# Optimization experiments

Hardware: AMD Instinct MI355X
Metric: run time of the kernel (lower is better)

Reference implementation:

```python
import jax, jax.numpy as jnp
import numpy as np

NUM_BEAMS = 2


def setup_inputs() -> dict:
    key = jax.random.key(0)
    ks = jax.random.split(key, 5)
    B, T, H, E, F = 128, 32, 768, 4, 3072
    x = jax.random.normal(ks[0], (B, T, H), dtype=jnp.float32)
    Wg = jax.random.normal(ks[1], (E, H), dtype=jnp.float32) * (1.0 / np.sqrt(H))
    W1 = jax.random.normal(ks[2], (E, H, F), dtype=jnp.float32) * (1.0 / np.sqrt(H))
    b1 = jnp.zeros((E, F), dtype=jnp.float32)
    W2 = jax.random.normal(ks[3], (E, F, H), dtype=jnp.float32) * (1.0 / np.sqrt(F))
    b2 = jnp.zeros((E, H), dtype=jnp.float32)
    return {"x": x, "Wg": Wg, "W1": W1, "b1": b1, "W2": W2, "b2": b2}


def reference(x, Wg, W1, b1, W2, b2):
    B, T, H = x.shape
    E = Wg.shape[0]
    nb = NUM_BEAMS
    # ---- forward_gate: mask is all-ones, so masked mean == mean over tokens ----
    x_avg = jnp.mean(x, axis=1)                          # [B, H]
    logits_gate = x_avg @ Wg.T                           # [B, E]
    prob_gate = jax.nn.softmax(logits_gate, axis=-1)     # [B, E]
    # ---- importance auxiliary loss (torch.std uses ddof=1) ----
    importance = jnp.sum(prob_gate, axis=0)              # [E]
    importance_loss = (jnp.std(importance, ddof=1) / jnp.mean(importance)) ** 2
    # ---- beam search, first layer: exp(log(p)) == p, top-k per row ----
    current_scores = jnp.exp(jnp.log(prob_gate))         # == prob_gate (kept for fidelity)
    topk_values, gate_idx = jax.lax.top_k(current_scores, nb)   # [B, nb]
    beam_scores = topk_values.reshape(nb * B)            # row-major flatten, matches .view
    expert_route = gate_idx.reshape(nb * B)[:, None]     # [B*nb, 1]
    beam_idx = jnp.arange(nb * B)
    current_expert_select = expert_route[:, -1]          # [B*nb]
    # ---- first layer: replicate x and scores along beam dim (interleaved) ----
    x_rep = jnp.repeat(x, nb, axis=0)                    # [B*nb, T, H]
    scores_rep = jnp.repeat(prob_gate, nb, axis=0)       # [B*nb, E]
    # input_x = x_rep[beam_idx] is identity here (beam_idx == arange)
    # ---- forward_expert_ffn: run ALL experts, mask+combine with gate prob ----
    h1 = jnp.einsum('bth,ehf->betf', x_rep, W1) + b1[None, :, None, :]
    h1 = jax.nn.gelu(h1, approximate=False)              # torch GELU is exact erf form
    cand = jnp.einsum('betf,efh->beth', h1, W2) + b2[None, :, None, :]  # [B*nb, E, T, H]
    weight = scores_rep * jax.nn.one_hot(current_expert_select, E, dtype=scores_rep.dtype)
    output = jnp.einsum('beth,be->bth', cand, weight)    # weighted sum over experts
    return output, beam_scores, expert_route, beam_idx, importance_loss
```

## Files before the change

### kernel.cpp

```cpp
#include <hip/hip_runtime.h>
#include <math.h>

typedef _Float16 f16;
typedef _Float16 f16x8 __attribute__((ext_vector_type(8)));
typedef float f32x4 __attribute__((ext_vector_type(4)));

#define Bn 128
#define Tn 32
#define Hn 768
#define En 4
#define Fn 3072
#define Rn 256
#define MAXT4 67

static constexpr size_t OUT_ELEMS  = (size_t)Rn*Tn*Hn;
static constexpr size_t SCORES_OFF = OUT_ELEMS;
static constexpr size_t ROUTE_OFF  = OUT_ELEMS + Rn;
static constexpr size_t BIDX_OFF   = OUT_ELEMS + 2*Rn;
static constexpr size_t LOSS_OFF   = OUT_ELEMS + 3*Rn;

#define WS_WSF    0u
#define WS_ROUTE  4096u
#define WS_GRP    8192u
#define WS_X16    16384u
#define WS_W1T    (WS_X16 + 2u*Bn*Tn*Hn)
#define WS_W2T    (WS_W1T + 2u*En*Hn*Fn)
#define WS_H1     (WS_W2T + 2u*En*Fn*Hn)

#define GLOAD16(g, l) __builtin_amdgcn_global_load_lds( \
    (const __attribute__((address_space(1))) unsigned int*)(g), \
    (__attribute__((address_space(3))) unsigned int*)(l), 16, 0, 0)

__device__ __forceinline__ float fast_gelu(float v) {
  float s = v * 0.70710678118f;
  float a = fabsf(s);
  float t = 1.0f / (1.0f + 0.3275911f * a);
  float y = t*(0.254829592f + t*(-0.284496736f + t*(1.421413741f +
            t*(-1.453152027f + t*1.061405429f))));
  float er = 1.0f - y * __expf(-a*a);
  er = (s < 0.0f) ? -er : er;
  return 0.5f * v * (1.0f + er);
}

__global__ __launch_bounds__(256) void gate_kernel(
    const float* __restrict__ x, const float* __restrict__ Wg,
    float* __restrict__ out, float* __restrict__ wsf, int* __restrict__ route,
    f16* __restrict__ x16)
{
  const int b = blockIdx.x;
  const int tid = threadIdx.x;
  const int w = tid >> 6, l = tid & 63;
  __shared__ float pacc[4][4];
  float a0=0.f, a1=0.f, a2=0.f, a3=0.f;
  const float* xb = x   + (size_t)b*Tn*Hn + (size_t)(w*8)*Hn;
  f16*         xh = x16 + (size_t)b*Tn*Hn + (size_t)(w*8)*Hn;
  #pragma unroll
  for (int k = 0; k < 12; ++k) {
    const int h = l + 64*k;
    const float w0 = Wg[0*Hn+h], w1 = Wg[1*Hn+h], w2 = Wg[2*Hn+h], w3 = Wg[3*Hn+h];
    #pragma unroll
    for (int t = 0; t < 8; ++t) {
      float v = xb[t*Hn + h];
      xh[t*Hn + h] = (f16)v;
      a0 += v*w0; a1 += v*w1; a2 += v*w2; a3 += v*w3;
    }
  }
  #pragma unroll
  for (int o = 32; o > 0; o >>= 1) {
    a0 += __shfl_down(a0,o); a1 += __shfl_down(a1,o);
    a2 += __shfl_down(a2,o); a3 += __shfl_down(a3,o);
  }
  if (l == 0) { pacc[w][0]=a0; pacc[w][1]=a1; pacc[w][2]=a2; pacc[w][3]=a3; }
  __syncthreads();
  if (tid == 0) {
    float lg[4];
    #pragma unroll
    for (int e = 0; e < 4; ++e)
      lg[e] = (pacc[0][e]+pacc[1][e]+pacc[2][e]+pacc[3][e]) * (1.0f/Tn);
    float m = fmaxf(fmaxf(lg[0],lg[1]), fmaxf(lg[2],lg[3]));
    float p[4]; float s = 0.f;
    #pragma unroll
    for (int e = 0; e < 4; ++e) { p[e] = expf(lg[e]-m); s += p[e]; }
    float inv = 1.f/s;
    #pragma unroll
    for (int e = 0; e < 4; ++e) { p[e] *= inv; wsf[b*4+e] = p[e]; }
    int i1 = 0;
    #pragma unroll
    for (int e = 1; e < 4; ++e) if (p[e] > p[i1]) i1 = e;
    int i2 = (i1 == 0) ? 1 : 0;
    #pragma unroll
    for (int e = 0; e < 4; ++e) if (e != i1 && p[e] > p[i2]) i2 = e;
    int idx[2] = {i1, i2};
    #pragma unroll
    for (int k = 0; k < 2; ++k) {
      int r = 2*b + k;
      float pv = p[idx[k]];
      wsf[512 + r] = pv;
      route[r] = idx[k];
      out[SCORES_OFF + r] = pv;
      out[ROUTE_OFF  + r] = (float)idx[k];
      out[BIDX_OFF   + r] = (float)r;
    }
  }
}

__global__ __launch_bounds__(64) void loss_kernel(
    const float* __restrict__ wsf, float* __restrict__ out)
{
  const int l = threadIdx.x;
  float i0=0.f,i1=0.f,i2=0.f,i3=0.f;
  for (int b = l; b < Bn; b += 64) {
    i0 += wsf[b*4+0]; i1 += wsf[b*4+1]; i2 += wsf[b*4+2]; i3 += wsf[b*4+3];
  }
  #pragma unroll
  for (int o = 32; o > 0; o >>= 1) {
    i0 += __shfl_down(i0,o); i1 += __shfl_down(i1,o);
    i2 += __shfl_down(i2,o); i3 += __shfl_down(i3,o);
  }
  if (l == 0) {
    float mean = 0.25f*(i0+i1+i2+i3);
    float d0=i0-mean, d1=i1-mean, d2=i2-mean, d3=i3-mean;
    float var = (d0*d0+d1*d1+d2*d2+d3*d3) * (1.f/3.f);
    out[LOSS_OFF] = var / (mean*mean);
  }
}

__global__ __launch_bounds__(64) void group_kernel(
    const int* __restrict__ route, int* __restrict__ grp)
{
  const int l = threadIdx.x;
  int cnt = 0;
  if (l < 4) { for (int r = 0; r < Rn; ++r) cnt += (route[r] == l); }
  int c0 = __shfl(cnt, 0), c1 = __shfl(cnt, 1), c2 = __shfl(cnt, 2), c3 = __shfl(cnt, 3);
  int off = (l >= 1 ? c0 : 0) + (l >= 2 ? c1 : 0) + (l >= 3 ? c2 : 0);
  if (l < 4) {
    int p = off;
    for (int r = 0; r < Rn; ++r) if (route[r] == l) grp[384 + p++] = r;
  }
  if (l == 0) {
    int cs[4] = {c0, c1, c2, c3};
    int os[4] = {0, c0, c0+c1, c0+c1+c2};
    int nt4 = 0;
    for (int e = 0; e < 4; ++e) {
      for (int s = 0; s < cs[e]; s += 4) {
        int nb = cs[e] - s; if (nb > 4) nb = 4;
        grp[8+nt4*3+0] = e; grp[8+nt4*3+1] = os[e]+s; grp[8+nt4*3+2] = nb;
        ++nt4;
      }
    }
    grp[0] = nt4;
  }
}

__global__ __launch_bounds__(256) void transcvt_kernel(
    const float* __restrict__ W1s, const float* __restrict__ W2s,
    f16* __restrict__ d1, f16* __restrict__ d2)
{
  __shared__ f16 t[64][74];
  int bid = blockIdx.x;
  const float* s; f16* d; int R, C, rc;
  if (bid < 2304) { s = W1s; d = d1; R = Hn; C = Fn; rc = bid; }
  else            { s = W2s; d = d2; R = Fn; C = Hn; rc = bid - 2304; }
  const int e = rc / 576; rc -= e*576;
  const int nx = C >> 6;
  const int cy = rc / nx, cx = rc - cy*nx;
  const int r0 = cy*64, c0 = cx*64;
  s += (size_t)e*R*C;
  d += (size_t)e*R*C;
  const int tid = threadIdx.x;
  const int i  = tid >> 2;
  const int j0 = (tid & 3) * 16;
  #pragma unroll
  for (int q = 0; q < 16; q += 4) {
    float4 v = *(const float4*)(s + (size_t)(r0+i)*C + c0 + j0 + q);
    t[i][j0+q+0]=(f16)v.x; t[i][j0+q+1]=(f16)v.y; t[i][j0+q+2]=(f16)v.z; t[i][j0+q+3]=(f16)v.w;
  }
  __syncthreads();
  f16 o[16];
  #pragma unroll
  for (int q = 0; q < 16; ++q) o[q] = t[j0+q][i];
  *(uint4*)(d + (size_t)(c0+i)*R + r0 + j0)     = *(uint4*)&o[0];
  *(uint4*)(d + (size_t)(c0+i)*R + r0 + j0 + 8) = *(uint4*)&o[8];
}

template<int KD, int ND, int BN, int NWAVE, bool G1>
__global__ __launch_bounds__(NWAVE*64, G1 ? 4 : 2) void gemm_kernel(
    const f16* __restrict__ A16, const f16* __restrict__ B16,
    const float* __restrict__ bias, f16* __restrict__ oh,
    float* __restrict__ of, const int* __restrict__ grp,
    const float* __restrict__ wsf)
{
  constexpr int NWY  = BN / 64;
  constexpr int NY   = ND / BN;
  constexpr int NT   = KD / 32;
  constexpr int NTHR = NWAVE * 64;
  constexpr int GL_A = 512 / NTHR;
  constexpr int GL_B = (BN*4) / NTHR;
  constexpr int NLD  = GL_A + GL_B;
  constexpr int BUFSZ = 8192 + BN*64;
  constexpr int TPR  = NWAVE * 2;
  static_assert(NT % 3 == 0, "NT%3");

  const int ntiles = grp[0];
  const int tix = blockIdx.x / NY;
  const int ny  = blockIdx.x % NY;
  if (tix >= ntiles) return;
  const int e      = grp[8+tix*3+0];
  const int bstart = grp[8+tix*3+1];
  const int nb     = grp[8+tix*3+2];
  const int n0     = ny * BN;
  const int tid    = threadIdx.x;
  const int lane   = tid & 63;
  const int w      = tid >> 6;

  extern __shared__ __align__(16) char smem[];

  const f16* asrc[GL_A];
  #pragma unroll
  for (int i = 0; i < GL_A; ++i) {
    const int U   = w*(GL_A*64) + i*64 + lane;
    const int row = U >> 2;
    const int gu  = (U & 3) ^ ((U >> 3) & 3);
    int slot = row >> 5; if (slot >= nb) slot = nb - 1;
    const int beam = grp[384 + bstart + slot];
    const size_t rbase = (G1 ? (size_t)(beam>>1)*Tn : (size_t)beam*Tn) + (row & 31);
    asrc[i] = A16 + rbase*(size_t)KD + gu*8;
  }
  const f16* bsrc[GL_B];
  #pragma unroll
  for (int i = 0; i < GL_B; ++i) {
    const int U   = w*(GL_B*64) + i*64 + lane;
    const int row = U >> 2;
    const int gu  = (U & 3) ^ ((U >> 3) & 3);
    bsrc[i] = B16 + (size_t)e*ND*KD + (size_t)(n0 + row)*KD + gu*8;
  }

  const int wm = w / NWY, wn = w % NWY;
  const int lr = lane & 15, lk = lane >> 4;
  const int rowA0 = wm*64;
  const int rowB0 = wn*64;
  const int ub = (lk ^ ((lr >> 1) & 3)) << 4;

  f32x4 acc[4][4];
  #pragma unroll
  for (int i=0;i<4;++i)
    #pragma unroll
    for (int j=0;j<4;++j) acc[i][j] = (f32x4){0.f,0.f,0.f,0.f};

  auto STAGE = [&](int bsel, int kt2) {
    char* Ad = smem + bsel*BUFSZ + (w*(GL_A*64))*16;
    #pragma unroll
    for (int i = 0; i < GL_A; ++i) GLOAD16(asrc[i] + kt2*32, Ad + i*1024);
    char* Bd = smem + bsel*BUFSZ + 8192 + (w*(GL_B*64))*16;
    #pragma unroll
    for (int i = 0; i < GL_B; ++i) GLOAD16(bsrc[i] + kt2*32, Bd + i*1024);
  };

  auto TILE = [&](int k, int b, bool dost, int vmc) {
    const char* Ab = smem + b*BUFSZ;
    const char* Bb = Ab + 8192;
    f16x8 af[4], bf[4];
    #pragma unroll
    for (int mi=0;mi<4;++mi)
      af[mi] = *(const f16x8*)(Ab + (rowA0 + mi*16 + lr)*64 + ub);
    #pragma unroll
    for (int ni=0;ni<4;++ni)
      bf[ni] = *(const f16x8*)(Bb + (rowB0 + ni*16 + lr)*64 + ub);
    if (dost) STAGE((b+2)%3, k+2);
    __builtin_amdgcn_sched_barrier(0);
    __builtin_amdgcn_s_barrier();
    __builtin_amdgcn_sched_barrier(0);
    asm volatile("s_waitcnt lgkmcnt(0)" ::: "memory");
    __builtin_amdgcn_sched_barrier(0);
    __builtin_amdgcn_s_setprio(1);
    #pragma unroll
    for (int mi=0;mi<4;++mi)
      #pragma unroll
      for (int ni=0;ni<4;++ni)
        acc[mi][ni] = __builtin_amdgcn_mfma_f32_16x16x32_f16(af[mi], bf[ni], acc[mi][ni], 0, 0, 0);
    __builtin_amdgcn_s_setprio(0);
    if (vmc > 0)       asm volatile("s_waitcnt vmcnt(%0)" :: "i"(NLD) : "memory");
    else if (vmc == 0) asm volatile("s_waitcnt vmcnt(0)" ::: "memory");
    __builtin_amdgcn_sched_barrier(0);
    __builtin_amdgcn_s_barrier();
    __builtin_amdgcn_sched_barrier(0);
  };

  STAGE(0, 0);
  STAGE(1, 1);
  asm volatile("s_waitcnt vmcnt(%0)" :: "i"(NLD) : "memory");
  __builtin_amdgcn_sched_barrier(0);
  __builtin_amdgcn_s_barrier();
  __builtin_amdgcn_sched_barrier(0);

  {
    int b = 0;
    for (int k = 0; k < NT-2; ++k) {
      TILE(k, b, true, NLD);
      b = (b+1)%3;
    }
    TILE(NT-2, b, false, 0);
    b = (b+1)%3;
    TILE(NT-1, b, false, -1);
  }

  const int nvalid = nb * Tn;
  char* cst = smem;
  float bvals[4];
  if (G1) {
    #pragma unroll
    for (int ni=0;ni<4;++ni) bvals[ni] = bias[e*ND + n0 + rowB0 + ni*16 + lr];
  }
  #pragma unroll
  for (int mi=0;mi<4;++mi){
    #pragma unroll
    for (int j=0;j<4;++j){
      const int m = rowA0 + mi*16 + (lane>>4)*4 + j;
      const int m7 = m & 7;
      #pragma unroll
      for (int ni=0;ni<4;++ni){
        const int n = rowB0 + ni*16 + lr;
        if (G1) {
          float v = acc[mi][ni][j] + bvals[ni];
          *(f16*)(cst + m*512 + (((n>>3)^m7)<<4) + (n&7)*2) = (f16)fast_gelu(v);
        } else {
          *(float*)(cst + m*512 + (((n>>2)^m7)<<4) + (n&3)*4) = acc[mi][ni][j];
        }
      }
    }
  }
  __syncthreads();
  {
    const int u  = tid & 31;
    const int tr = tid >> 5;
    float4 b4;
    if (!G1) b4 = *(const float4*)(bias + e*ND + n0 + u*4);
    #pragma unroll
    for (int it = 0; it < 128/TPR; ++it) {
      const int rl = it*TPR + tr;
      if (rl < nvalid) {
        const int beam = grp[384 + bstart + (rl>>5)];
        if (G1) {
          uint4 v = *(const uint4*)(cst + rl*512 + (((u&24)|((u&7)^(rl&7)))<<4));
          *(uint4*)(oh + ((size_t)beam*Tn + (rl&31))*(size_t)ND + n0 + u*8) = v;
        } else {
          const float sc = wsf[512 + beam];
          float4 v = *(const float4*)(cst + rl*512 + (((u&24)|((u&7)^(rl&7)))<<4));
          v.x = (v.x + b4.x)*sc; v.y = (v.y + b4.y)*sc;
          v.z = (v.z + b4.z)*sc; v.w = (v.w + b4.w)*sc;
          *(float4*)(of + ((size_t)beam*Tn + (rl&31))*(size_t)Hn + n0 + u*4) = v;
        }
      }
    }
  }
}

extern "C" void kernel_launch(void* const* d_in, const int* in_sizes, int n_in,
                              void* d_out, int out_size, void* d_ws, size_t ws_size,
                              hipStream_t stream)
{
  const float* x  = (const float*)d_in[0];
  const float* Wg = (const float*)d_in[1];
  const float* W1 = (const float*)d_in[2];
  const float* b1 = (const float*)d_in[3];
  const float* W2 = (const float*)d_in[4];
  const float* b2 = (const float*)d_in[5];
  float* out = (float*)d_out;
  char* ws = (char*)d_ws;
  float* wsf  = (float*)(ws + WS_WSF);
  int*   route= (int*)(ws + WS_ROUTE);
  int*   grp  = (int*)(ws + WS_GRP);
  f16*   x16  = (f16*)(ws + WS_X16);
  f16*   w1t  = (f16*)(ws + WS_W1T);
  f16*   w2t  = (f16*)(ws + WS_W2T);
  f16*   h1   = (f16*)(ws + WS_H1);

  gate_kernel<<<Bn, 256, 0, stream>>>(x, Wg, out, wsf, route, x16);
  group_kernel<<<1, 64, 0, stream>>>(route, grp);
  loss_kernel<<<1, 64, 0, stream>>>(wsf, out);
  transcvt_kernel<<<4608, 256, 0, stream>>>(W1, W2, w1t, w2t);

  auto g1 = gemm_kernel<Hn, Fn, 256, 8, true>;
  auto g2 = gemm_kernel<Fn, Hn, 128, 4, false>;
  const int sm1 = 3*(8192 + 256*64);
  const int sm2 = 65536;
  hipFuncSetAttribute((const void*)g1, hipFuncAttributeMaxDynamicSharedMemorySize, sm1);
  hipFuncSetAttribute((const void*)g2, hipFuncAttributeMaxDynamicSharedMemorySize, sm2);
  g1<<<MAXT4*12, 512, sm1, stream>>>(x16, w1t, b1, h1, nullptr, grp, wsf);
  g2<<<MAXT4*6,  256, sm2, stream>>>(h1, w2t, b2, nullptr, out, grp, wsf);
}
```

Measured before the change: 204.7 us.

## Shrink GEMM tiles, switch to double-buffered pipeline, reorder grid by column tile

Both grouped-expert GEMMs now use 256-thread blocks with smaller N tiles (128 for the first, 64 for the second), so more blocks launch and more can be resident per CU at lower LDS use. The three-stage prefetch pipeline with priority hints becomes a simpler two-buffer scheme that waits for all loads before every barrier. Block indexing now iterates row tiles fastest, so blocks sharing a weight column tile run close together. The epilogue is split into two halves to fit the smaller shared buffer. In exchange, less load latency is hidden per block and each A tile is re-read from global memory more times.

```diff
diff --git a/kernel.cpp b/kernel.cpp
--- a/kernel.cpp
+++ b/kernel.cpp
@@ -183,27 +183,21 @@
   *(uint4*)(d + (size_t)(c0+i)*R + r0 + j0 + 8) = *(uint4*)&o[8];
 }
 
-template<int KD, int ND, int BN, int NWAVE, bool G1>
-__global__ __launch_bounds__(NWAVE*64, G1 ? 4 : 2) void gemm_kernel(
+template<int KD, int ND, int BN, int NI, bool G1>
+__global__ __launch_bounds__(256, 4) void gemm_kernel(
     const f16* __restrict__ A16, const f16* __restrict__ B16,
     const float* __restrict__ bias, f16* __restrict__ oh,
     float* __restrict__ of, const int* __restrict__ grp,
     const float* __restrict__ wsf)
 {
-  constexpr int NWY  = BN / 64;
-  constexpr int NY   = ND / BN;
   constexpr int NT   = KD / 32;
-  constexpr int NTHR = NWAVE * 64;
-  constexpr int GL_A = 512 / NTHR;
-  constexpr int GL_B = (BN*4) / NTHR;
-  constexpr int NLD  = GL_A + GL_B;
-  constexpr int BUFSZ = 8192 + BN*64;
-  constexpr int TPR  = NWAVE * 2;
-  static_assert(NT % 3 == 0, "NT%3");
+  constexpr int GL_B = BN / 64;
+  constexpr int BUFSZ = (128 + BN) * 64;
+  static_assert(NT % 2 == 0, "NT even");
 
   const int ntiles = grp[0];
-  const int tix = blockIdx.x / NY;
-  const int ny  = blockIdx.x % NY;
+  const int ny  = blockIdx.x / MAXT4;
+  const int tix = blockIdx.x % MAXT4;
   if (tix >= ntiles) return;
   const int e      = grp[8+tix*3+0];
   const int bstart = grp[8+tix*3+1];
@@ -215,10 +209,10 @@
 
   extern __shared__ __align__(16) char smem[];
 
-  const f16* asrc[GL_A];
-  #pragma unroll
-  for (int i = 0; i < GL_A; ++i) {
-    const int U   = w*(GL_A*64) + i*64 + lane;
+  const f16* asrc[2];
+  #pragma unroll
+  for (int i = 0; i < 2; ++i) {
+    const int U   = w*128 + i*64 + lane;
     const int row = U >> 2;
     const int gu  = (U & 3) ^ ((U >> 3) & 3);
     int slot = row >> 5; if (slot >= nb) slot = nb - 1;
@@ -235,123 +229,118 @@
     bsrc[i] = B16 + (size_t)e*ND*KD + (size_t)(n0 + row)*KD + gu*8;
   }
 
-  const int wm = w / NWY, wn = w % NWY;
+  const int wm = w >> 1, wn = w & 1;
   const int lr = lane & 15, lk = lane >> 4;
   const int rowA0 = wm*64;
-  const int rowB0 = wn*64;
+  const int rowB0 = wn*(NI*16);
   const int ub = (lk ^ ((lr >> 1) & 3)) << 4;
 
-  f32x4 acc[4][4];
+  f32x4 acc[4][NI];
   #pragma unroll
   for (int i=0;i<4;++i)
     #pragma unroll
-    for (int j=0;j<4;++j) acc[i][j] = (f32x4){0.f,0.f,0.f,0.f};
+    for (int j=0;j<NI;++j) acc[i][j] = (f32x4){0.f,0.f,0.f,0.f};
 
   auto STAGE = [&](int bsel, int kt2) {
-    char* Ad = smem + bsel*BUFSZ + (w*(GL_A*64))*16;
-    #pragma unroll
-    for (int i = 0; i < GL_A; ++i) GLOAD16(asrc[i] + kt2*32, Ad + i*1024);
+    char* Ad = smem + bsel*BUFSZ + (w*128)*16;
+    #pragma unroll
+    for (int i = 0; i < 2; ++i) GLOAD16(asrc[i] + kt2*32, Ad + i*1024);
     char* Bd = smem + bsel*BUFSZ + 8192 + (w*(GL_B*64))*16;
     #pragma unroll
     for (int i = 0; i < GL_B; ++i) GLOAD16(bsrc[i] + kt2*32, Bd + i*1024);
   };
 
-  auto TILE = [&](int k, int b, bool dost, int vmc) {
+  auto TILE = [&](int k, int b) {
     const char* Ab = smem + b*BUFSZ;
     const char* Bb = Ab + 8192;
-    f16x8 af[4], bf[4];
+    f16x8 af[4], bf[NI];
     #pragma unroll
     for (int mi=0;mi<4;++mi)
       af[mi] = *(const f16x8*)(Ab + (rowA0 + mi*16 + lr)*64 + ub);
     #pragma unroll
-    for (int ni=0;ni<4;++ni)
+    for (int ni=0;ni<NI;++ni)
       bf[ni] = *(const f16x8*)(Bb + (rowB0 + ni*16 + lr)*64 + ub);
-    if (dost) STAGE((b+2)%3, k+2);
-    __builtin_amdgcn_sched_barrier(0);
-    __builtin_amdgcn_s_barrier();
-    __builtin_amdgcn_sched_barrier(0);
+    if (k + 1 < NT) STAGE(b ^ 1, k + 1);
     asm volatile("s_waitcnt lgkmcnt(0)" ::: "memory");
     __builtin_amdgcn_sched_barrier(0);
-    __builtin_amdgcn_s_setprio(1);
     #pragma unroll
     for (int mi=0;mi<4;++mi)
       #pragma unroll
-      for (int ni=0;ni<4;++ni)
+      for (int ni=0;ni<NI;++ni)
         acc[mi][ni] = __builtin_amdgcn_mfma_f32_16x16x32_f16(af[mi], bf[ni], acc[mi][ni], 0, 0, 0);
-    __builtin_amdgcn_s_setprio(0);
-    if (vmc > 0)       asm volatile("s_waitcnt vmcnt(%0)" :: "i"(NLD) : "memory");
-    else if (vmc == 0) asm volatile("s_waitcnt vmcnt(0)" ::: "memory");
+    asm volatile("s_waitcnt vmcnt(0)" ::: "memory");
     __builtin_amdgcn_sched_barrier(0);
     __builtin_amdgcn_s_barrier();
     __builtin_amdgcn_sched_barrier(0);
   };
 
   STAGE(0, 0);
-  STAGE(1, 1);
-  asm volatile("s_waitcnt vmcnt(%0)" :: "i"(NLD) : "memory");
+  asm volatile("s_waitcnt vmcnt(0)" ::: "memory");
   __builtin_amdgcn_sched_barrier(0);
   __builtin_amdgcn_s_barrier();
   __builtin_amdgcn_sched_barrier(0);
 
-  {
-    int b = 0;
-    for (int k = 0; k < NT-2; ++k) {
-      TILE(k, b, true, NLD);
-      b = (b+1)%3;
-    }
-    TILE(NT-2, b, false, 0);
-    b = (b+1)%3;
-    TILE(NT-1, b, false, -1);
+  for (int k = 0; k < NT; k += 2) {
+    TILE(k,   0);
+    TILE(k+1, 1);
   }
 
   const int nvalid = nb * Tn;
   char* cst = smem;
-  float bvals[4];
-  if (G1) {
-    #pragma unroll
-    for (int ni=0;ni<4;++ni) bvals[ni] = bias[e*ND + n0 + rowB0 + ni*16 + lr];
-  }
-  #pragma unroll
-  for (int mi=0;mi<4;++mi){
-    #pragma unroll
-    for (int j=0;j<4;++j){
-      const int m = rowA0 + mi*16 + (lane>>4)*4 + j;
-      const int m7 = m & 7;
+  float bvals[NI];
+  #pragma unroll
+  for (int ni=0;ni<NI;++ni)
+    if (G1) bvals[ni] = bias[e*ND + n0 + rowB0 + ni*16 + lr];
+
+  #pragma unroll
+  for (int h = 0; h < 2; ++h) {
+    if (wm == h) {
       #pragma unroll
-      for (int ni=0;ni<4;++ni){
-        const int n = rowB0 + ni*16 + lr;
-        if (G1) {
-          float v = acc[mi][ni][j] + bvals[ni];
-          *(f16*)(cst + m*512 + (((n>>3)^m7)<<4) + (n&7)*2) = (f16)fast_gelu(v);
-        } else {
-          *(float*)(cst + m*512 + (((n>>2)^m7)<<4) + (n&3)*4) = acc[mi][ni][j];
+      for (int mi=0;mi<4;++mi){
+        #pragma unroll
+        for (int j=0;j<4;++j){
+          const int m = mi*16 + (lane>>4)*4 + j;
+          const int m7 = m & 7;
+          #pragma unroll
+          for (int ni=0;ni<NI;++ni){
+            const int n = rowB0 + ni*16 + lr;
+            if (G1) {
+              float v = acc[mi][ni][j] + bvals[ni];
+              *(f16*)(cst + m*512 + (((n>>3)^m7)<<4) + (n&7)*2) = (f16)fast_gelu(v);
+            } else {
+              *(float*)(cst + m*512 + (((n>>2)^m7)<<4) + (n&3)*4) = acc[mi][ni][j];
+            }
+          }
         }
       }
     }
-  }
-  __syncthreads();
-  {
-    const int u  = tid & 31;
-    const int tr = tid >> 5;
-    float4 b4;
-    if (!G1) b4 = *(const float4*)(bias + e*ND + n0 + u*4);
-    #pragma unroll
-    for (int it = 0; it < 128/TPR; ++it) {
-      const int rl = it*TPR + tr;
-      if (rl < nvalid) {
-        const int beam = grp[384 + bstart + (rl>>5)];
-        if (G1) {
-          uint4 v = *(const uint4*)(cst + rl*512 + (((u&24)|((u&7)^(rl&7)))<<4));
-          *(uint4*)(oh + ((size_t)beam*Tn + (rl&31))*(size_t)ND + n0 + u*8) = v;
-        } else {
-          const float sc = wsf[512 + beam];
-          float4 v = *(const float4*)(cst + rl*512 + (((u&24)|((u&7)^(rl&7)))<<4));
-          v.x = (v.x + b4.x)*sc; v.y = (v.y + b4.y)*sc;
-          v.z = (v.z + b4.z)*sc; v.w = (v.w + b4.w)*sc;
-          *(float4*)(of + ((size_t)beam*Tn + (rl&31))*(size_t)Hn + n0 + u*4) = v;
+    __syncthreads();
+    {
+      const int u  = tid & 15;
+      const int tr = tid >> 4;
+      float4 b4;
+      if (!G1) b4 = *(const float4*)(bias + e*ND + n0 + u*4);
+      #pragma unroll
+      for (int it = 0; it < 4; ++it) {
+        const int rl = it*16 + tr;
+        const int r  = h*64 + rl;
+        if (r < nvalid) {
+          const int beam = grp[384 + bstart + (r>>5)];
+          const char* src = cst + rl*512 + ((u ^ (rl&7))<<4);
+          if (G1) {
+            uint4 v = *(const uint4*)src;
+            *(uint4*)(oh + ((size_t)beam*Tn + (r&31))*(size_t)ND + n0 + u*8) = v;
+          } else {
+            const float sc = wsf[512 + beam];
+            float4 v = *(const float4*)src;
+            v.x = (v.x + b4.x)*sc; v.y = (v.y + b4.y)*sc;
+            v.z = (v.z + b4.z)*sc; v.w = (v.w + b4.w)*sc;
+            *(float4*)(of + ((size_t)beam*Tn + (r&31))*(size_t)Hn + n0 + u*4) = v;
+          }
         }
       }
     }
+    __syncthreads();
   }
 }
 
@@ -380,12 +369,11 @@
   loss_kernel<<<1, 64, 0, stream>>>(wsf, out);
   transcvt_kernel<<<4608, 256, 0, stream>>>(W1, W2, w1t, w2t);
 
-  auto g1 = gemm_kernel<Hn, Fn, 256, 8, true>;
-  auto g2 = gemm_kernel<Fn, Hn, 128, 4, false>;
-  const int sm1 = 3*(8192 + 256*64);
-  const int sm2 = 65536;
-  hipFuncSetAttribute((const void*)g1, hipFuncAttributeMaxDynamicSharedMemorySize, sm1);
-  hipFuncSetAttribute((const void*)g2, hipFuncAttributeMaxDynamicSharedMemorySize, sm2);
-  g1<<<MAXT4*12, 512, sm1, stream>>>(x16, w1t, b1, h1, nullptr, grp, wsf);
-  g2<<<MAXT4*6,  256, sm2, stream>>>(h1, w2t, b2, nullptr, out, grp, wsf);
-}
+  auto g1 = gemm_kernel<Hn, Fn, 128, 4, true>;
+  auto g2 = gemm_kernel<Fn, Hn,  64, 2, false>;
+  const int smB = 32768;
+  hipFuncSetAttribute((const void*)g1, hipFuncAttributeMaxDynamicSharedMemorySize, smB);
+  hipFuncSetAttribute((const void*)g2, hipFuncAttributeMaxDynamicSharedMemorySize, smB);
+  g1<<<24*MAXT4, 256, smB, stream>>>(x16, w1t, b1, h1, nullptr, grp, wsf);
+  g2<<<12*MAXT4, 256, smB, stream>>>(h1, w2t, b2, nullptr, out, grp, wsf);
+}
```

Result: slower. 270.5 us (+32.2%).

## Use 256x256 tiles with 8-beam groups and split-phase pipeline for first GEMM

Applied to the files above, without the earlier changes.

The first expert GEMM gets its own kernel that takes 256-row tiles (up to 8 beams per group) by 256 columns, with a K-step of 64 and double-buffered 128KB LDS. Each wave computes a 128x64 sub-tile in four MFMA phases, with loads for the next stages interleaved between the phases. The grouping kernel now emits separate 8-beam and 4-beam tile lists for the two GEMMs. This cuts how often the W1 tiles are reloaded and raises arithmetic intensity, but it costs more padding waste for partial groups and lower occupancy from the large LDS footprint.

```diff
diff --git a/kernel.cpp b/kernel.cpp
--- a/kernel.cpp
+++ b/kernel.cpp
@@ -11,6 +11,7 @@
 #define En 4
 #define Fn 3072
 #define Rn 256
+#define MAXT8 35
 #define MAXT4 67
 
 static constexpr size_t OUT_ELEMS  = (size_t)Rn*Tn*Hn;
@@ -30,6 +31,9 @@
 #define GLOAD16(g, l) __builtin_amdgcn_global_load_lds( \
     (const __attribute__((address_space(1))) unsigned int*)(g), \
     (__attribute__((address_space(3))) unsigned int*)(l), 16, 0, 0)
+
+#define SBAR()  __builtin_amdgcn_s_barrier()
+#define SCHED() __builtin_amdgcn_sched_barrier(0)
 
 __device__ __forceinline__ float fast_gelu(float v) {
   float s = v * 0.70710678118f;
@@ -140,15 +144,21 @@
   if (l == 0) {
     int cs[4] = {c0, c1, c2, c3};
     int os[4] = {0, c0, c0+c1, c0+c1+c2};
-    int nt4 = 0;
+    int nt8 = 0, nt4 = 0;
     for (int e = 0; e < 4; ++e) {
+      for (int s = 0; s < cs[e]; s += 8) {
+        int nb = cs[e] - s; if (nb > 8) nb = 8;
+        grp[8+nt8*3+0] = e; grp[8+nt8*3+1] = os[e]+s; grp[8+nt8*3+2] = nb;
+        ++nt8;
+      }
       for (int s = 0; s < cs[e]; s += 4) {
         int nb = cs[e] - s; if (nb > 4) nb = 4;
-        grp[8+nt4*3+0] = e; grp[8+nt4*3+1] = os[e]+s; grp[8+nt4*3+2] = nb;
+        grp[128+nt4*3+0] = e; grp[128+nt4*3+1] = os[e]+s; grp[128+nt4*3+2] = nb;
         ++nt4;
       }
     }
-    grp[0] = nt4;
+    grp[0] = nt8;
+    grp[1] = nt4;
   }
 }
 
@@ -183,12 +193,170 @@
   *(uint4*)(d + (size_t)(c0+i)*R + r0 + j0 + 8) = *(uint4*)&o[8];
 }
 
-template<int KD, int ND, int BN, int NWAVE, bool G1>
-__global__ __launch_bounds__(NWAVE*64, G1 ? 4 : 2) void gemm_kernel(
+__global__ __launch_bounds__(512) void gemm1_kernel(
     const f16* __restrict__ A16, const f16* __restrict__ B16,
     const float* __restrict__ bias, f16* __restrict__ oh,
-    float* __restrict__ of, const int* __restrict__ grp,
-    const float* __restrict__ wsf)
+    const int* __restrict__ grp)
+{
+  constexpr int KD = Hn, ND = Fn, NT = KD/64, NY = Fn/256;
+  const int ntiles = grp[0];
+  const int tix = blockIdx.x / NY;
+  const int ny  = blockIdx.x % NY;
+  if (tix >= ntiles) return;
+  const int e      = grp[8+tix*3+0];
+  const int bstart = grp[8+tix*3+1];
+  const int nb     = grp[8+tix*3+2];
+  const int n0     = ny * 256;
+  const int tid    = threadIdx.x;
+  const int lane   = tid & 63;
+  const int w      = tid >> 6;
+
+  extern __shared__ __align__(16) char smem[];
+
+  const f16* aS[2][2];
+  const f16* bS[2][2];
+  #pragma unroll
+  for (int h = 0; h < 2; ++h) {
+    #pragma unroll
+    for (int i = 0; i < 2; ++i) {
+      const int U = w*128 + i*64 + lane;
+      const int r128 = U >> 3;
+      const int gu = (U & 7) ^ (r128 & 7);
+      const int rowA = h*128 + r128;
+      int slot = rowA >> 5; if (slot >= nb) slot = nb - 1;
+      const int beam = grp[384 + bstart + slot];
+      aS[h][i] = A16 + ((size_t)(beam>>1)*Tn + (rowA&31))*(size_t)KD + gu*8;
+      bS[h][i] = B16 + (size_t)e*ND*KD + (size_t)(n0 + h*128 + r128)*KD + gu*8;
+    }
+  }
+
+  const int wm = w >> 2, wn = w & 3;
+  const int lr = lane & 15, lk = lane >> 4;
+  const int r7 = lr & 7;
+  const char* Abase = smem + wm*16384;
+  const char* Bbase = smem + 32768 + (wn>>1)*16384;
+  const int cb = (wn & 1) * 64;
+
+  f32x4 acc[8][4];
+  #pragma unroll
+  for (int i=0;i<8;++i)
+    #pragma unroll
+    for (int j=0;j<4;++j) acc[i][j] = (f32x4){0.f,0.f,0.f,0.f};
+
+  auto STAGE_A = [&](int d, int h, int kt) {
+    char* dst = smem + d*65536 + h*16384 + w*2048;
+    GLOAD16(aS[h][0] + kt*64, dst);
+    GLOAD16(aS[h][1] + kt*64, dst + 1024);
+  };
+  auto STAGE_B = [&](int d, int h, int kt) {
+    char* dst = smem + d*65536 + 32768 + h*16384 + w*2048;
+    GLOAD16(bS[h][0] + kt*64, dst);
+    GLOAD16(bS[h][1] + kt*64, dst + 1024);
+  };
+
+  f16x8 af[4][2], bf[2][2][2];
+
+#define LDA(MH, MI, KS) \
+  *(const f16x8*)(Abase + d*65536 + ((MH)*64 + (MI)*16 + lr)*128 + (((KS)*4+lk)^r7)*16)
+#define LDB(NH, NI, KS) \
+  *(const f16x8*)(Bbase + d*65536 + (cb + (NH)*32 + (NI)*16 + lr)*128 + (((KS)*4+lk)^r7)*16)
+#define MFMA16(MH, NH) \
+  __builtin_amdgcn_s_setprio(1); \
+  _Pragma("unroll") \
+  for (int mi=0;mi<4;++mi) \
+    _Pragma("unroll") \
+    for (int ni=0;ni<2;++ni) \
+      _Pragma("unroll") \
+      for (int ks=0;ks<2;++ks) \
+        acc[(MH)*4+mi][(NH)*2+ni] = __builtin_amdgcn_mfma_f32_16x16x32_f16( \
+            af[mi][ks], bf[NH][ni][ks], acc[(MH)*4+mi][(NH)*2+ni], 0, 0, 0); \
+  __builtin_amdgcn_s_setprio(0);
+
+  STAGE_A(0,0,0); STAGE_A(0,1,0); STAGE_B(0,0,0); STAGE_B(0,1,0);
+  STAGE_A(1,0,1); STAGE_A(1,1,1); STAGE_B(1,0,1); STAGE_B(1,1,1);
+  asm volatile("s_waitcnt vmcnt(8)" ::: "memory");
+  SCHED(); SBAR(); SCHED();
+
+  for (int kt = 0; kt < NT; ++kt) {
+    const int d = kt & 1;
+    const bool st = (kt + 2 < NT);
+    #pragma unroll
+    for (int mi=0;mi<4;++mi) { af[mi][0] = LDA(0,mi,0); af[mi][1] = LDA(0,mi,1); }
+    #pragma unroll
+    for (int ni=0;ni<2;++ni) { bf[0][ni][0] = LDB(0,ni,0); bf[0][ni][1] = LDB(0,ni,1); }
+    SBAR(); SCHED();
+    asm volatile("s_waitcnt lgkmcnt(0)" ::: "memory");
+    SCHED();
+    MFMA16(0,0);
+    SBAR(); SCHED();
+    #pragma unroll
+    for (int ni=0;ni<2;++ni) { bf[1][ni][0] = LDB(1,ni,0); bf[1][ni][1] = LDB(1,ni,1); }
+    SBAR(); SCHED();
+    asm volatile("s_waitcnt lgkmcnt(0)" ::: "memory");
+    SCHED();
+    MFMA16(0,1);
+    SBAR(); SCHED();
+    #pragma unroll
+    for (int mi=0;mi<4;++mi) { af[mi][0] = LDA(1,mi,0); af[mi][1] = LDA(1,mi,1); }
+    if (st) { STAGE_B(d, 0, kt+2); STAGE_B(d, 1, kt+2); }
+    SBAR(); SCHED();
+    asm volatile("s_waitcnt lgkmcnt(0)" ::: "memory");
+    SCHED();
+    MFMA16(1,0);
+    SBAR(); SCHED();
+    if (st) { STAGE_A(d, 0, kt+2); STAGE_A(d, 1, kt+2); }
+    SBAR(); SCHED();
+    MFMA16(1,1);
+    if (st)                asm volatile("s_waitcnt vmcnt(8)" ::: "memory");
+    else if (kt + 1 < NT)  asm volatile("s_waitcnt vmcnt(0)" ::: "memory");
+    SCHED(); SBAR(); SCHED();
+  }
+#undef LDA
+#undef LDB
+#undef MFMA16
+
+  __syncthreads();
+  const int nvalid = nb * Tn;
+  char* cst = smem;
+  float bvals[4];
+  #pragma unroll
+  for (int ni=0;ni<4;++ni) bvals[ni] = bias[e*ND + n0 + wn*64 + ni*16 + lr];
+
+  #pragma unroll
+  for (int mi=0;mi<8;++mi){
+    #pragma unroll
+    for (int j=0;j<4;++j){
+      const int m = wm*128 + mi*16 + (lane>>4)*4 + j;
+      const int m7 = m & 7;
+      #pragma unroll
+      for (int ni=0;ni<4;++ni){
+        const int n = wn*64 + ni*16 + lr;
+        float v = acc[mi][ni][j] + bvals[ni];
+        *(f16*)(cst + m*512 + (((n>>3)^m7)<<4) + (n&7)*2) = (f16)fast_gelu(v);
+      }
+    }
+  }
+  __syncthreads();
+  {
+    const int u  = tid & 31;
+    const int tr = tid >> 5;
+    #pragma unroll
+    for (int it = 0; it < 16; ++it) {
+      const int r = it*16 + tr;
+      if (r < nvalid) {
+        const int beam = grp[384 + bstart + (r>>5)];
+        uint4 v = *(const uint4*)(cst + r*512 + (((u&24)|((u&7)^(r&7)))<<4));
+        *(uint4*)(oh + ((size_t)beam*Tn + (r&31))*(size_t)ND + n0 + u*8) = v;
+      }
+    }
+  }
+}
+
+template<int KD, int ND, int BN, int NWAVE>
+__global__ __launch_bounds__(NWAVE*64, 2) void gemm2_kernel(
+    const f16* __restrict__ A16, const f16* __restrict__ B16,
+    const float* __restrict__ bias, float* __restrict__ of,
+    const int* __restrict__ grp, const float* __restrict__ wsf)
 {
   constexpr int NWY  = BN / 64;
   constexpr int NY   = ND / BN;
@@ -201,13 +369,13 @@
   constexpr int TPR  = NWAVE * 2;
   static_assert(NT % 3 == 0, "NT%3");
 
-  const int ntiles = grp[0];
+  const int ntiles = grp[1];
   const int tix = blockIdx.x / NY;
   const int ny  = blockIdx.x % NY;
   if (tix >= ntiles) return;
-  const int e      = grp[8+tix*3+0];
-  const int bstart = grp[8+tix*3+1];
-  const int nb     = grp[8+tix*3+2];
+  const int e      = grp[128+tix*3+0];
+  const int bstart = grp[128+tix*3+1];
+  const int nb     = grp[128+tix*3+2];
   const int n0     = ny * BN;
   const int tid    = threadIdx.x;
   const int lane   = tid & 63;
@@ -223,7 +391,7 @@
     const int gu  = (U & 3) ^ ((U >> 3) & 3);
     int slot = row >> 5; if (slot >= nb) slot = nb - 1;
     const int beam = grp[384 + bstart + slot];
-    const size_t rbase = (G1 ? (size_t)(beam>>1)*Tn : (size_t)beam*Tn) + (row & 31);
+    const size_t rbase = (size_t)beam*Tn + (row & 31);
     asrc[i] = A16 + rbase*(size_t)KD + gu*8;
   }
   const f16* bsrc[GL_B];
@@ -267,11 +435,9 @@
     for (int ni=0;ni<4;++ni)
       bf[ni] = *(const f16x8*)(Bb + (rowB0 + ni*16 + lr)*64 + ub);
     if (dost) STAGE((b+2)%3, k+2);
-    __builtin_amdgcn_sched_barrier(0);
-    __builtin_amdgcn_s_barrier();
-    __builtin_amdgcn_sched_barrier(0);
+    SCHED(); SBAR(); SCHED();
     asm volatile("s_waitcnt lgkmcnt(0)" ::: "memory");
-    __builtin_amdgcn_sched_barrier(0);
+    SCHED();
     __builtin_amdgcn_s_setprio(1);
     #pragma unroll
     for (int mi=0;mi<4;++mi)
@@ -281,17 +447,13 @@
     __builtin_amdgcn_s_setprio(0);
     if (vmc > 0)       asm volatile("s_waitcnt vmcnt(%0)" :: "i"(NLD) : "memory");
     else if (vmc == 0) asm volatile("s_waitcnt vmcnt(0)" ::: "memory");
-    __builtin_amdgcn_sched_barrier(0);
-    __builtin_amdgcn_s_barrier();
-    __builtin_amdgcn_sched_barrier(0);
+    SCHED(); SBAR(); SCHED();
   };
 
   STAGE(0, 0);
   STAGE(1, 1);
   asm volatile("s_waitcnt vmcnt(%0)" :: "i"(NLD) : "memory");
-  __builtin_amdgcn_sched_barrier(0);
-  __builtin_amdgcn_s_barrier();
-  __builtin_amdgcn_sched_barrier(0);
+  SCHED(); SBAR(); SCHED();
 
   {
     int b = 0;
@@ -306,11 +468,6 @@
 
   const int nvalid = nb * Tn;
   char* cst = smem;
-  float bvals[4];
-  if (G1) {
-    #pragma unroll
-    for (int ni=0;ni<4;++ni) bvals[ni] = bias[e*ND + n0 + rowB0 + ni*16 + lr];
-  }
   #pragma unroll
   for (int mi=0;mi<4;++mi){
     #pragma unroll
@@ -320,12 +477,7 @@
       #pragma unroll
       for (int ni=0;ni<4;++ni){
         const int n = rowB0 + ni*16 + lr;
-        if (G1) {
-          float v = acc[mi][ni][j] + bvals[ni];
-          *(f16*)(cst + m*512 + (((n>>3)^m7)<<4) + (n&7)*2) = (f16)fast_gelu(v);
-        } else {
-          *(float*)(cst + m*512 + (((n>>2)^m7)<<4) + (n&3)*4) = acc[mi][ni][j];
-        }
+        *(float*)(cst + m*512 + (((n>>2)^m7)<<4) + (n&3)*4) = acc[mi][ni][j];
       }
     }
   }
@@ -333,23 +485,17 @@
   {
     const int u  = tid & 31;
     const int tr = tid >> 5;
-    float4 b4;
-    if (!G1) b4 = *(const float4*)(bias + e*ND + n0 + u*4);
+    float4 b4 = *(const float4*)(bias + e*ND + n0 + u*4);
     #pragma unroll
     for (int it = 0; it < 128/TPR; ++it) {
       const int rl = it*TPR + tr;
       if (rl < nvalid) {
         const int beam = grp[384 + bstart + (rl>>5)];
-        if (G1) {
-          uint4 v = *(const uint4*)(cst + rl*512 + (((u&24)|((u&7)^(rl&7)))<<4));
-          *(uint4*)(oh + ((size_t)beam*Tn + (rl&31))*(size_t)ND + n0 + u*8) = v;
-        } else {
-          const float sc = wsf[512 + beam];
-          float4 v = *(const float4*)(cst + rl*512 + (((u&24)|((u&7)^(rl&7)))<<4));
-          v.x = (v.x + b4.x)*sc; v.y = (v.y + b4.y)*sc;
-          v.z = (v.z + b4.z)*sc; v.w = (v.w + b4.w)*sc;
-          *(float4*)(of + ((size_t)beam*Tn + (rl&31))*(size_t)Hn + n0 + u*4) = v;
-        }
+        const float sc = wsf[512 + beam];
+        float4 v = *(const float4*)(cst + rl*512 + (((u&24)|((u&7)^(rl&7)))<<4));
+        v.x = (v.x + b4.x)*sc; v.y = (v.y + b4.y)*sc;
+        v.z = (v.z + b4.z)*sc; v.w = (v.w + b4.w)*sc;
+        *(float4*)(of + ((size_t)beam*Tn + (rl&31))*(size_t)Hn + n0 + u*4) = v;
       }
     }
   }
@@ -380,12 +526,11 @@
   loss_kernel<<<1, 64, 0, stream>>>(wsf, out);
   transcvt_kernel<<<4608, 256, 0, stream>>>(W1, W2, w1t, w2t);
 
-  auto g1 = gemm_kernel<Hn, Fn, 256, 8, true>;
-  auto g2 = gemm_kernel<Fn, Hn, 128, 4, false>;
-  const int sm1 = 3*(8192 + 256*64);
+  auto g2 = gemm2_kernel<Fn, Hn, 128, 4>;
+  const int sm1 = 131072;
   const int sm2 = 65536;
-  hipFuncSetAttribute((const void*)g1, hipFuncAttributeMaxDynamicSharedMemorySize, sm1);
+  hipFuncSetAttribute((const void*)gemm1_kernel, hipFuncAttributeMaxDynamicSharedMemorySize, sm1);
   hipFuncSetAttribute((const void*)g2, hipFuncAttributeMaxDynamicSharedMemorySize, sm2);
-  g1<<<MAXT4*12, 512, sm1, stream>>>(x16, w1t, b1, h1, nullptr, grp, wsf);
-  g2<<<MAXT4*6,  256, sm2, stream>>>(h1, w2t, b2, nullptr, out, grp, wsf);
-}
+  gemm1_kernel<<<MAXT8*12, 512, sm1, stream>>>(x16, w1t, b1, h1, grp);
+  g2<<<MAXT4*6, 256, sm2, stream>>>(h1, w2t, b2, out, grp, wsf);
+}
```

After: 212.0 us. 1.04x slower.
